# Kernel optimization log

Measured on AMD Instinct MI355X. Metric: run time of the kernel, lower is better.

The kernel has to match this reference:

```python
import jax, jax.numpy as jnp
import numpy as np
from jax import lax

B, T, D, H, L = 128, 512, 256, 256, 2


def setup_inputs() -> dict:
    key = jax.random.key(0)
    ks = jax.random.split(key, 8)
    s = 1.0 / np.sqrt(H)
    return {
        "input1": jax.random.normal(ks[0], (B, T, D), jnp.float32),
        "input2": jax.random.normal(ks[1], (B, T, D), jnp.float32),
        "W_ih": jax.random.normal(ks[2], (L, 4 * H, D), jnp.float32) * s,
        "W_hh": jax.random.normal(ks[3], (L, 4 * H, H), jnp.float32) * s,
        "b_ih": jax.random.normal(ks[4], (L, 4 * H), jnp.float32) * s,
        "b_hh": jax.random.normal(ks[5], (L, 4 * H), jnp.float32) * s,
        "fc_w": jax.random.normal(ks[6], (5, H), jnp.float32) * s,
        "fc_b": jax.random.normal(ks[7], (5,), jnp.float32) * s,
    }


def _lstm_layer(x, Wih, Whh, bih, bhh):
    # x: [B, T, in]; returns (outputs [B, T, H], final h [B, H])
    b = x.shape[0]
    # precompute input projection for all timesteps (one big GEMM)
    xg = jnp.einsum('bti,gi->btg', x, Wih) + bih + bhh  # [B, T, 4H]
    h0 = jnp.zeros((b, H), x.dtype)
    c0 = jnp.zeros((b, H), x.dtype)

    def step(carry, xg_t):
        h, c = carry
        gates = xg_t + h @ Whh.T  # [B, 4H]
        i, f, g, o = jnp.split(gates, 4, axis=-1)
        i = jax.nn.sigmoid(i)
        f = jax.nn.sigmoid(f)
        g = jnp.tanh(g)
        o = jax.nn.sigmoid(o)
        c = f * c + i * g
        h = o * jnp.tanh(c)
        return (h, c), h

    (h_last, _), hs = lax.scan(step, (h0, c0), jnp.swapaxes(xg, 0, 1))
    return jnp.swapaxes(hs, 0, 1), h_last


def _forward_once(x, W_ih, W_hh, b_ih, b_hh, fc_w, fc_b):
    h_finals = []
    out = x
    for l in range(L):
        out, h_last = _lstm_layer(out, W_ih[l], W_hh[l], b_ih[l], b_hh[l])
        h_finals.append(h_last)
    hn = jnp.stack(h_finals, axis=0).reshape(-1, H)  # [L*B, H] (torch hn.view)
    return jax.nn.relu(hn) @ fc_w.T + fc_b  # [L*B, 5]


def reference(input1, input2, W_ih, W_hh, b_ih, b_hh, fc_w, fc_b):
    out1 = _forward_once(input1, W_ih, W_hh, b_ih, b_hh, fc_w, fc_b)
    out2 = _forward_once(input2, W_ih, W_hh, b_ih, b_hh, fc_w, fc_b)
    return (out1, out2)
```

## Files before the change

### kernel.cpp

```cpp
#include <hip/hip_runtime.h>
#include <hip/hip_fp16.h>

typedef unsigned int  u32;
typedef unsigned short u16;

typedef _Float16 h2v __attribute__((ext_vector_type(2)));
typedef _Float16 h8v __attribute__((ext_vector_type(8)));
typedef float    f4v __attribute__((ext_vector_type(4)));

static __device__ __forceinline__ u16 f2h_bits(float x){
    _Float16 h = (_Float16)x;
    return __builtin_bit_cast(u16, h);
}
static __device__ __forceinline__ u32 pack2(float a, float b){
    return (u32)f2h_bits(a) | ((u32)f2h_bits(b) << 16);
}
static __device__ __forceinline__ float fdot2(u32 w, u32 h, float acc){
#if __has_builtin(__builtin_amdgcn_fdot2)
    return __builtin_amdgcn_fdot2(__builtin_bit_cast(h2v, w),
                                  __builtin_bit_cast(h2v, h), acc, false);
#else
    h2v wv = __builtin_bit_cast(h2v, w), hv = __builtin_bit_cast(h2v, h);
    return acc + (float)wv[0]*(float)hv[0] + (float)wv[1]*(float)hv[1];
#endif
}
template<int CTRL>
static __device__ __forceinline__ float dpp_qp(float x){
#if __has_builtin(__builtin_amdgcn_mov_dpp)
    int r = __builtin_amdgcn_mov_dpp(__builtin_bit_cast(int, x), CTRL, 0xF, 0xF, true);
    return __builtin_bit_cast(float, r);
#else
    return __shfl_xor(x, (CTRL == 0xB1) ? 1 : 2);
#endif
}


__global__ void cvt_weights(const float* __restrict__ Wih,
                            const float* __restrict__ Whh,
                            const float* __restrict__ bih,
                            const float* __restrict__ bhh,
                            u32* __restrict__ wih16u,
                            u32* __restrict__ wreg,
                            u32* __restrict__ wldsg,
                            float* __restrict__ bias){
    u32 e = blockIdx.x * blockDim.x + threadIdx.x;
    {
        float2 v = ((const float2*)Wih)[e];
        wih16u[e] = pack2(v.x, v.y);
    }
    if (e < 196608u){
        u32 l = (e >= 98304u) ? 1u : 0u;
        u32 rem = e - l*98304u;
        u32 pidx = rem >> 10, L = rem & 1023u;
        u32 r = pidx / 24u, p = pidx - r*24u;
        u32 j = L >> 2, q = L & 3u;
        u32 row = r*256u + j;
        u32 P = 32u*q + p;
        float2 v = ((const float2*)Whh)[((size_t)l*1024u + row)*128u + P];
        wreg[e] = pack2(v.x, v.y);
    } else {
        u32 e2 = e - 196608u;
        u32 l = e2 >> 15, rem = e2 & 32767u;
        u32 i2 = rem >> 10, L = rem & 1023u;
        u32 r = i2 >> 3, k = i2 & 7u;
        u32 j = L >> 2, q = L & 3u;
        u32 row = r*256u + j;
        u32 P = 32u*q + 24u + k;
        float2 v = ((const float2*)Whh)[((size_t)l*1024u + row)*128u + P];
        wldsg[e2] = pack2(v.x, v.y);
    }
    if (e < 2048u){
        u32 l = e >> 10, Ls = e & 1023u;
        u32 src = l*1024u + (((Ls & 3u) << 8) | (Ls >> 2));
        bias[e] = bih[src] + bhh[src];
    }
}

template<int A_FP32>
__global__ __launch_bounds__(256) void proj_gemm(
        const float* __restrict__ in1, const float* __restrict__ in2,
        const u16*  __restrict__ A16,
        const u16*  __restrict__ Bw,
        u16*        __restrict__ Cout,
        int t0, int lgTc){
    __shared__ u16 Blds[128][264];
    const int tid = threadIdx.x;
    const int n0 = blockIdx.x * 128;
    const int m0 = blockIdx.y * 128;

    {
        const u32* src = (const u32*)Bw;
        #pragma unroll
        for (int i = 0; i < 64; i++){
            int idx = i*256 + tid;
            int r  = idx >> 7;
            int cu = idx & 127;
            u32 v = src[(size_t)(n0 + r)*128 + cu];
            *(u32*)&Blds[r][cu*2] = v;
        }
    }
    __syncthreads();

    const int l   = tid & 63;
    const int wid = tid >> 6;
    const int wm = (wid >> 1) * 64;
    const int wn = (wid & 1) * 64;
    const int lr = l & 15;
    const int lk = l >> 4;

    f4v acc[4][4] = {};

    const float* a32[4];
    const u16*   a16[4];
    #pragma unroll
    for (int f = 0; f < 4; f++){
        int m = m0 + wm + f*16 + lr;
        if (A_FP32){
            int beta = m >> lgTc;
            int tc   = m & ((1 << lgTc) - 1);
            const float* base = (beta < 128) ? in1 : in2;
            a32[f] = base + ((size_t)(beta & 127)*512 + (size_t)(t0 + tc))*256 + lk*8;
        } else {
            a16[f] = A16 + (size_t)m*256 + lk*8;
        }
    }

    #pragma unroll
    for (int ks = 0; ks < 8; ks++){
        uint4 a_[4], b_[4];
        #pragma unroll
        for (int f = 0; f < 4; f++){
            if (A_FP32){
                float4 v0 = *(const float4*)(a32[f] + ks*32);
                float4 v1 = *(const float4*)(a32[f] + ks*32 + 4);
                a_[f] = make_uint4(pack2(v0.x, v0.y), pack2(v0.z, v0.w),
                                   pack2(v1.x, v1.y), pack2(v1.z, v1.w));
            } else {
                a_[f] = *(const uint4*)(a16[f] + ks*32);
            }
        }
        #pragma unroll
        for (int f = 0; f < 4; f++)
            b_[f] = *(const uint4*)&Blds[wn + f*16 + lr][ks*32 + lk*8];
        #pragma unroll
        for (int fm = 0; fm < 4; fm++)
            #pragma unroll
            for (int fn = 0; fn < 4; fn++)
                acc[fm][fn] = __builtin_amdgcn_mfma_f32_16x16x32_f16(
                    __builtin_bit_cast(h8v, a_[fm]),
                    __builtin_bit_cast(h8v, b_[fn]),
                    acc[fm][fn], 0, 0, 0);
    }

    #pragma unroll
    for (int fm = 0; fm < 4; fm++){
        #pragma unroll
        for (int i = 0; i < 4; i++){
            int m = m0 + wm + fm*16 + lk*4 + i;
            size_t rowoff = (size_t)m*1024;
            #pragma unroll
            for (int fn = 0; fn < 4; fn++){
                int n = n0 + wn + fn*16 + lr;
                int np = ((n & 255) << 2) | (n >> 8);
                Cout[rowoff + np] = f2h_bits(acc[fm][fn][i]);
            }
        }
    }
}

__global__ __launch_bounds__(1024, 4) void lstm_rec(
        const u16* __restrict__ xg,
        const u32* __restrict__ wreg,
        const u32* __restrict__ wldsg,
        const float* __restrict__ bias,
        u16* __restrict__ hseq,
        u16* __restrict__ h_state,
        float* __restrict__ c_state,
        int Tc, int write_seq, int first){
    __shared__ u32 wlds[1024*36];
    __shared__ alignas(16) u16 hbufF[2*288];

    const int L    = threadIdx.x;
    const int q    = L & 3;
    const int j    = L >> 2;
    const int beta = blockIdx.x;

    u32 w[96];
    #pragma unroll
    for (int t = 0; t < 96; t++)
        w[t] = wreg[(size_t)t*1024 + L];
    #pragma unroll
    for (int i = 0; i < 32; i++)
        wlds[L*36 + i] = wldsg[(size_t)i*1024 + L];

    const float bs = bias[L];
    float c = 0.f;
    u16 hb_last = 0;
    if (q == 0){
        u16 h0 = first ? (u16)0 : h_state[(size_t)beta*256 + j];
        hbufF[72*(j >> 6) + (j & 63)] = h0;
        hb_last = h0;
        if (!first) c = c_state[(size_t)beta*256 + j];
    }
    __syncthreads();

    const u16* xr = xg + (size_t)beta * Tc * 1024 + L;
    u16 xcur = xr[0];
    const uint4* wr = (const uint4*)&wlds[L*36];

    for (int tc = 0; tc < Tc; tc++){
        u16 xnext = (tc + 1 < Tc) ? xr[(size_t)(tc+1)*1024] : (u16)0;

        const uint4* hv = (const uint4*)&hbufF[(tc & 1)*288 + 72*q];
        float pA = 0.f, pB = 0.f, pC = 0.f, pD = 0.f;

        #pragma unroll
        for (int i = 0; i < 6; i++){
            uint4 hh = hv[i];
            pA = fdot2(w[   4*i+0], hh.x, pA); pA = fdot2(w[   4*i+1], hh.y, pA);
            pA = fdot2(w[   4*i+2], hh.z, pA); pA = fdot2(w[   4*i+3], hh.w, pA);
            pB = fdot2(w[24+4*i+0], hh.x, pB); pB = fdot2(w[24+4*i+1], hh.y, pB);
            pB = fdot2(w[24+4*i+2], hh.z, pB); pB = fdot2(w[24+4*i+3], hh.w, pB);
            pC = fdot2(w[48+4*i+0], hh.x, pC); pC = fdot2(w[48+4*i+1], hh.y, pC);
            pC = fdot2(w[48+4*i+2], hh.z, pC); pC = fdot2(w[48+4*i+3], hh.w, pC);
            pD = fdot2(w[72+4*i+0], hh.x, pD); pD = fdot2(w[72+4*i+1], hh.y, pD);
            pD = fdot2(w[72+4*i+2], hh.z, pD); pD = fdot2(w[72+4*i+3], hh.w, pD);
        }
        #pragma unroll
        for (int m = 0; m < 2; m++){
            uint4 hh = hv[6+m];
            uint4 wa = wr[0+m], wb = wr[2+m], wc = wr[4+m], wd = wr[6+m];
            pA = fdot2(wa.x, hh.x, pA); pA = fdot2(wa.y, hh.y, pA);
            pA = fdot2(wa.z, hh.z, pA); pA = fdot2(wa.w, hh.w, pA);
            pB = fdot2(wb.x, hh.x, pB); pB = fdot2(wb.y, hh.y, pB);
            pB = fdot2(wb.z, hh.z, pB); pB = fdot2(wb.w, hh.w, pB);
            pC = fdot2(wc.x, hh.x, pC); pC = fdot2(wc.y, hh.y, pC);
            pC = fdot2(wc.z, hh.z, pC); pC = fdot2(wc.w, hh.w, pC);
            pD = fdot2(wd.x, hh.x, pD); pD = fdot2(wd.y, hh.y, pD);
            pD = fdot2(wd.z, hh.z, pD); pD = fdot2(wd.w, hh.w, pD);
        }

        float k0_ = (q & 1) ? pB : pA;
        float k1_ = (q & 1) ? pD : pC;
        float s0_ = (q & 1) ? pA : pB;
        float s1_ = (q & 1) ? pC : pD;
        k0_ += dpp_qp<0xB1>(s0_);
        k1_ += dpp_qp<0xB1>(s1_);
        float kf = (q & 2) ? k1_ : k0_;
        float sf = (q & 2) ? k0_ : k1_;
        kf += dpp_qp<0x4E>(sf);

        float acc = kf + bs + (float)__builtin_bit_cast(_Float16, xcur);

        float targ = (q == 2) ? 2.f*acc : -acc;
        float e1 = __expf(targ);
        float rr = 1.f / (1.f + e1);
        float a  = (q == 2) ? 1.f - 2.f*rr : rr;

        float p1 = dpp_qp<0xB1>(a);
        float p2 = dpp_qp<0x4E>(a);
        float p3 = dpp_qp<0x4E>(p1);

        c = (q == 0) ? (p1*c + a*p2) : 0.f;
        float e2 = __expf(2.f*c);
        float th = 1.f - 2.f/(e2 + 1.f);
        float h  = p3 * th;
        u16 hb = f2h_bits(h);

        if (q == 0){
            hbufF[((tc & 1)^1)*288 + 72*(j >> 6) + (j & 63)] = hb;
            hb_last = hb;
            if (write_seq) hseq[((size_t)beta*Tc + tc)*256 + j] = hb;
        }
        xcur = xnext;
        __syncthreads();
    }

    if (q == 0){
        h_state[(size_t)beta*256 + j] = hb_last;
        c_state[(size_t)beta*256 + j] = c;
    }
}

__global__ void fc_out(const u16* __restrict__ hlast,
                       const float* __restrict__ fcw,
                       const float* __restrict__ fcb,
                       float* __restrict__ out){
    int r = blockIdx.x;
    int lane = threadIdx.x;
    int inp = r >> 8, rem = r & 255, l = rem >> 7, b = rem & 127;
    int beta = inp*128 + b;
    const u16* h = hlast + ((size_t)l*256 + beta)*256;

    int j0 = lane * 4;
    uint2 hb = *(const uint2*)(h + j0);
    h2v p0 = __builtin_bit_cast(h2v, hb.x), p1 = __builtin_bit_cast(h2v, hb.y);
    float hv0 = fmaxf((float)p0[0], 0.f);
    float hv1 = fmaxf((float)p0[1], 0.f);
    float hv2 = fmaxf((float)p1[0], 0.f);
    float hv3 = fmaxf((float)p1[1], 0.f);

    float acc[5];
    #pragma unroll
    for (int k = 0; k < 5; k++){
        float4 w = *(const float4*)(fcw + k*256 + j0);
        acc[k] = hv0*w.x + hv1*w.y + hv2*w.z + hv3*w.w;
    }
    #pragma unroll
    for (int k = 0; k < 5; k++)
        #pragma unroll
        for (int off = 32; off > 0; off >>= 1)
            acc[k] += __shfl_xor(acc[k], off);
    if (lane == 0){
        #pragma unroll
        for (int k = 0; k < 5; k++)
            out[(size_t)r*5 + k] = acc[k] + fcb[k];
    }
}

extern "C" void kernel_launch(void* const* d_in, const int* in_sizes, int n_in,
                              void* d_out, int out_size, void* d_ws, size_t ws_size,
                              hipStream_t stream) {
    const float* in1 = (const float*)d_in[0];
    const float* in2 = (const float*)d_in[1];
    const float* Wih = (const float*)d_in[2];
    const float* Whh = (const float*)d_in[3];
    const float* bih = (const float*)d_in[4];
    const float* bhh = (const float*)d_in[5];
    const float* fcw = (const float*)d_in[6];
    const float* fcb = (const float*)d_in[7];
    float* out = (float*)d_out;

    char* ws = (char*)d_ws;
    u16*   wih16   = (u16*)  (ws + 0x000000);
    u32*   wreg    = (u32*)  (ws + 0x100000);
    u32*   wldsg   = (u32*)  (ws + 0x1C0000);
    float* bias    = (float*)(ws + 0x200000);
    u16*   h_state = (u16*)  (ws + 0x202000);
    float* c_state = (float*)(ws + 0x242000);
    const size_t chunk_off = 0x300000;

    int Tc = 8;
    for (int cand = 512; cand >= 8; cand >>= 1){
        if (chunk_off + (size_t)cand * 655360ull <= ws_size){ Tc = cand; break; }
    }
    int lgTc = 31 - __builtin_clz((u32)Tc);
    u16* xgc = (u16*)(ws + chunk_off);
    u16* hsc = (u16*)(ws + chunk_off + (size_t)Tc * 524288ull);

    cvt_weights<<<1024, 256, 0, stream>>>(Wih, Whh, bih, bhh,
                                          (u32*)wih16, wreg, wldsg, bias);

    const int nch = 512 / Tc;
    dim3 pg(8, 2*Tc);
    for (int k = 0; k < nch; k++){
        int t0 = k * Tc;
        proj_gemm<1><<<pg, 256, 0, stream>>>(in1, in2, (const u16*)nullptr,
                                             wih16, xgc, t0, lgTc);
        lstm_rec<<<256, 1024, 0, stream>>>((const u16*)xgc, wreg, wldsg, bias,
                                           hsc, h_state, c_state,
                                           Tc, 1, k == 0);
        proj_gemm<0><<<pg, 256, 0, stream>>>((const float*)nullptr, (const float*)nullptr,
                                             (const u16*)hsc,
                                             wih16 + 262144, xgc, 0, lgTc);
        lstm_rec<<<256, 1024, 0, stream>>>((const u16*)xgc, wreg + 98304, wldsg + 32768,
                                           bias + 1024,
                                           (u16*)nullptr, h_state + 65536, c_state + 65536,
                                           Tc, 0, k == 0);
    }
    fc_out<<<512, 64, 0, stream>>>(h_state, fcw, fcb, out);
}
```

Before: 2.476 ms.

## Pre-convert input chunk to fp16 and simplify projection GEMM loads

Adds a separate kernel that converts each fp32 input chunk to fp16 into the hs buffer, so the layer-0 projection GEMM reads fp16 A tiles like layer 1 and the template variant goes away. The grid is transposed so blockIdx.x walks M tiles, and the B-tile LDS fill uses 16-byte loads instead of 4-byte ones. Without the split, each of the 8 N-tile blocks re-read and re-converted the same fp32 rows. The cost is an extra launch per chunk and an extra fp16 write and read of the chunk.

```diff
diff --git a/kernel.cpp b/kernel.cpp
--- a/kernel.cpp
+++ b/kernel.cpp
@@ -76,27 +76,37 @@
     }
 }
 
-template<int A_FP32>
+__global__ void cvt_chunk(const float* __restrict__ in1,
+                          const float* __restrict__ in2,
+                          u16* __restrict__ a16,
+                          int t0, int lgTc){
+    u32 idx = blockIdx.x * blockDim.x + threadIdx.x;
+    u32 c4  = idx & 63;
+    u32 row = idx >> 6;
+    u32 tc   = row & ((1u << lgTc) - 1u);
+    u32 beta = row >> lgTc;
+    const float* base = (beta < 128u) ? in1 : in2;
+    float4 v = *(const float4*)(base + ((size_t)(beta & 127u)*512u + (size_t)(t0 + tc))*256u + c4*4u);
+    ((uint2*)a16)[idx] = make_uint2(pack2(v.x, v.y), pack2(v.z, v.w));
+}
+
 __global__ __launch_bounds__(256) void proj_gemm(
-        const float* __restrict__ in1, const float* __restrict__ in2,
         const u16*  __restrict__ A16,
         const u16*  __restrict__ Bw,
-        u16*        __restrict__ Cout,
-        int t0, int lgTc){
+        u16*        __restrict__ Cout){
     __shared__ u16 Blds[128][264];
     const int tid = threadIdx.x;
-    const int n0 = blockIdx.x * 128;
-    const int m0 = blockIdx.y * 128;
+    const int m0 = blockIdx.x * 128;
+    const int n0 = blockIdx.y * 128;
 
     {
-        const u32* src = (const u32*)Bw;
-        #pragma unroll
-        for (int i = 0; i < 64; i++){
+        const uint4* src = (const uint4*)Bw;
+        #pragma unroll
+        for (int i = 0; i < 16; i++){
             int idx = i*256 + tid;
-            int r  = idx >> 7;
-            int cu = idx & 127;
-            u32 v = src[(size_t)(n0 + r)*128 + cu];
-            *(u32*)&Blds[r][cu*2] = v;
+            int r = idx >> 5, c4 = idx & 31;
+            uint4 v = src[(size_t)(n0 + r)*32 + c4];
+            *(uint4*)&Blds[r][c4*8] = v;
         }
     }
     __syncthreads();
@@ -110,35 +120,17 @@
 
     f4v acc[4][4] = {};
 
-    const float* a32[4];
-    const u16*   a16[4];
-    #pragma unroll
-    for (int f = 0; f < 4; f++){
-        int m = m0 + wm + f*16 + lr;
-        if (A_FP32){
-            int beta = m >> lgTc;
-            int tc   = m & ((1 << lgTc) - 1);
-            const float* base = (beta < 128) ? in1 : in2;
-            a32[f] = base + ((size_t)(beta & 127)*512 + (size_t)(t0 + tc))*256 + lk*8;
-        } else {
-            a16[f] = A16 + (size_t)m*256 + lk*8;
-        }
-    }
+    const u16* a16p[4];
+    #pragma unroll
+    for (int f = 0; f < 4; f++)
+        a16p[f] = A16 + (size_t)(m0 + wm + f*16 + lr)*256 + lk*8;
 
     #pragma unroll
     for (int ks = 0; ks < 8; ks++){
         uint4 a_[4], b_[4];
         #pragma unroll
-        for (int f = 0; f < 4; f++){
-            if (A_FP32){
-                float4 v0 = *(const float4*)(a32[f] + ks*32);
-                float4 v1 = *(const float4*)(a32[f] + ks*32 + 4);
-                a_[f] = make_uint4(pack2(v0.x, v0.y), pack2(v0.z, v0.w),
-                                   pack2(v1.x, v1.y), pack2(v1.z, v1.w));
-            } else {
-                a_[f] = *(const uint4*)(a16[f] + ks*32);
-            }
-        }
+        for (int f = 0; f < 4; f++)
+            a_[f] = *(const uint4*)(a16p[f] + ks*32);
         #pragma unroll
         for (int f = 0; f < 4; f++)
             b_[f] = *(const uint4*)&Blds[wn + f*16 + lr][ks*32 + lk*8];
@@ -352,17 +344,15 @@
                                           (u32*)wih16, wreg, wldsg, bias);
 
     const int nch = 512 / Tc;
-    dim3 pg(8, 2*Tc);
+    dim3 pg(2*Tc, 8);
     for (int k = 0; k < nch; k++){
         int t0 = k * Tc;
-        proj_gemm<1><<<pg, 256, 0, stream>>>(in1, in2, (const u16*)nullptr,
-                                             wih16, xgc, t0, lgTc);
+        cvt_chunk<<<64*Tc, 256, 0, stream>>>(in1, in2, hsc, t0, lgTc);
+        proj_gemm<<<pg, 256, 0, stream>>>(hsc, wih16, xgc);
         lstm_rec<<<256, 1024, 0, stream>>>((const u16*)xgc, wreg, wldsg, bias,
                                            hsc, h_state, c_state,
                                            Tc, 1, k == 0);
-        proj_gemm<0><<<pg, 256, 0, stream>>>((const float*)nullptr, (const float*)nullptr,
-                                             (const u16*)hsc,
-                                             wih16 + 262144, xgc, 0, lgTc);
+        proj_gemm<<<pg, 256, 0, stream>>>(hsc, wih16 + 262144, xgc);
         lstm_rec<<<256, 1024, 0, stream>>>((const u16*)xgc, wreg + 98304, wldsg + 32768,
                                            bias + 1024,
                                            (u16*)nullptr, h_state + 65536, c_state + 65536,
```

New measurement: 2.376 ms. 4.1% less time.
